# Kernel tuning notes

Hardware: AMD Instinct MI355X
Metric: run time of the kernel (lower is better)

The kernel has to match this reference:

```python
import jax, jax.numpy as jnp
import numpy as np
import math

B, S, D, H = 2, 2048, 1024, 16
HD = D // H  # 64


def setup_inputs() -> dict:
    key = jax.random.key(0)
    ks = jax.random.split(key, 12)
    s = 1.0 / math.sqrt(D)
    inp = {
        "x": jax.random.normal(ks[0], (B, S, D), dtype=jnp.float32),
        "Wq": jax.random.normal(ks[1], (D, D), dtype=jnp.float32) * s,
        "bq": jnp.zeros((D,), dtype=jnp.float32),
        "Wk": jax.random.normal(ks[2], (D, D), dtype=jnp.float32) * s,
        "bk": jnp.zeros((D,), dtype=jnp.float32),
        "Wv": jax.random.normal(ks[3], (D, D), dtype=jnp.float32) * s,
        "bv": jnp.zeros((D,), dtype=jnp.float32),
        "Wo": jax.random.normal(ks[4], (D, D), dtype=jnp.float32) * s,
        "bo": jnp.zeros((D,), dtype=jnp.float32),
        "cross_modal_weights": jnp.ones((3, 3), dtype=jnp.float32),
        "mask": jax.random.randint(ks[5], (B, S, S), 0, 2, dtype=jnp.int32),
        "modality_info": jax.random.randint(ks[6], (B, S), 0, 3, dtype=jnp.int64),
    }
    return inp


def reference(x, Wq, bq, Wk, bk, Wv, bv, Wo, bo, cross_modal_weights, mask, modality_info):
    b, s, d = x.shape
    # QKV projections -> [b, H, s, HD]
    q = (x @ Wq + bq).reshape(b, s, H, HD).transpose(0, 2, 1, 3)
    k = (x @ Wk + bk).reshape(b, s, H, HD).transpose(0, 2, 1, 3)
    v = (x @ Wv + bv).reshape(b, s, H, HD).transpose(0, 2, 1, 3)
    scores = jnp.einsum("bhqd,bhkd->bhqk", q, k) / math.sqrt(HD)
    # modality bias: torch uses .item() -> detached scalar
    modality_bias = jax.lax.stop_gradient(jnp.mean(cross_modal_weights))
    scores = scores + modality_bias
    # user mask [b, s, s] broadcast over heads; masked_fill(mask==0, -1e9)
    scores = jnp.where(mask[:, None, :, :] == 0, jnp.float32(-1e9), scores)
    attn = jax.nn.softmax(scores, axis=-1)
    # dropout_rate = 0.0 (eval) -> identity
    ctx = jnp.einsum("bhqk,bhkd->bhqd", attn, v)
    ctx = ctx.transpose(0, 2, 1, 3).reshape(b, s, d)
    return ctx @ Wo + bo
```

## Files before the change

### kernel.cpp

```cpp
#include <hip/hip_runtime.h>
#include <math.h>

#define Bdim 2
#define Sdim 2048
#define Ddim 1024
#define Hnum 16
#define HDdim 64
#define Kdim 1024

using short8   = __attribute__((ext_vector_type(8))) short;
using ushort8  = __attribute__((ext_vector_type(8))) unsigned short;
using ushort4v = __attribute__((ext_vector_type(4))) unsigned short;
using floatx4  = __attribute__((ext_vector_type(4))) float;
using half4    = __attribute__((ext_vector_type(4))) _Float16;
using half2v   = __attribute__((ext_vector_type(2))) _Float16;

__device__ __forceinline__ unsigned short f2bf(float f) {
    __bf16 b = (__bf16)f;
    return __builtin_bit_cast(unsigned short, b);
}

__device__ __forceinline__ void async_ld16(const unsigned short* g, unsigned short* l) {
    __builtin_amdgcn_global_load_lds(
        (const __attribute__((address_space(1))) unsigned int*)(g),
        (__attribute__((address_space(3))) unsigned int*)(l), 16, 0, 0);
}

__global__ __launch_bounds__(256) void prep_kernel(
    const float* __restrict__ x,
    const float* __restrict__ Wq, const float* __restrict__ Wk,
    const float* __restrict__ Wv, const float* __restrict__ Wo,
    const int* __restrict__ mask,
    unsigned short* __restrict__ xb, unsigned short* __restrict__ Wt,
    unsigned long long* __restrict__ packed)
{
    __shared__ float tile[64][65];
    const int bid = blockIdx.x;
    const int t   = threadIdx.x;

    if (bid < 2048) {
        size_t i = ((size_t)bid * 256 + t) * 8;
        float4 a = *(const float4*)(x + i);
        float4 b = *(const float4*)(x + i + 4);
        ushort8 o;
        o[0] = f2bf(a.x); o[1] = f2bf(a.y); o[2] = f2bf(a.z); o[3] = f2bf(a.w);
        o[4] = f2bf(b.x); o[5] = f2bf(b.y); o[6] = f2bf(b.z); o[7] = f2bf(b.w);
        *(ushort8*)(xb + i) = o;
    } else if (bid < 3072) {
        const int idx = bid - 2048;
        const int n0 = (idx & 15) * 64;
        const int k0 = ((idx >> 4) & 15) * 64;
        const int z  = idx >> 8;
        const float* W = (z == 0) ? Wq : (z == 1) ? Wk : (z == 2) ? Wv : Wo;
        unsigned short* outp = Wt + (size_t)z * Kdim * Ddim;
#pragma unroll
        for (int i = 0; i < 4; ++i) {
            int flat = i * 256 + t;
            int r = flat >> 4;
            int c = (flat & 15) * 4;
            float4 v = *(const float4*)(W + (size_t)(k0 + r) * Ddim + n0 + c);
            tile[r][c] = v.x; tile[r][c+1] = v.y; tile[r][c+2] = v.z; tile[r][c+3] = v.w;
        }
        __syncthreads();
#pragma unroll
        for (int i = 0; i < 16; ++i) {
            int flat = i * 256 + t;
            int n = flat >> 6;
            int k = flat & 63;
            outp[(size_t)(n0 + n) * Kdim + k0 + k] = f2bf(tile[k][n]);
        }
    } else {
        const int lane = t & 63;
        const int l15  = lane & 15;
        const int quad = lane >> 4;
        const unsigned int gid = (bid - 3072) * 4 + (t >> 6);
        const int b  = gid >> 14;
        const int qg = (gid >> 7) & 127;
        const int kb = gid & 127;
        int4 mv = *(const int4*)(mask + ((size_t)(b * Sdim) + qg * 16 + l15) * Sdim + kb * 16 + quad * 4);
        unsigned long long w0 = __ballot(mv.x != 0);
        unsigned long long w1 = __ballot(mv.y != 0);
        unsigned long long w2 = __ballot(mv.z != 0);
        unsigned long long w3 = __ballot(mv.w != 0);
        if (lane == 0) {
            unsigned long long* dst = packed + (size_t)gid * 4;
            dst[0] = w0; dst[1] = w1; dst[2] = w2; dst[3] = w3;
        }
    }
}

#define MFMA_NORM(MT, NT) acc[MT][NT] = __builtin_amdgcn_mfma_f32_16x16x32_bf16(af[MT], bfr[NT], acc[MT][NT], 0, 0, 0)
#define MFMA_SWAP(MT, NT) acc[MT][NT] = __builtin_amdgcn_mfma_f32_16x16x32_bf16(bfr[NT], af[MT], acc[MT][NT], 0, 0, 0)

#define GEMM_KLOOP(APTR, WPTR, NT_TILES, MFMA_STMT)                              \
    for (int kt = 0; kt < 16; ++kt) {                                            \
        const int k0 = kt * 64;                                                  \
        __syncthreads();                                                         \
        _Pragma("unroll")                                                        \
        for (int i = 0; i < 4; ++i) {                                            \
            int flat = i * 256 + t;                                              \
            int row  = flat >> 3;                                                \
            int cg   = (flat & 7) ^ (row & 7);                                   \
            async_ld16(APTR + (size_t)(m0 + row) * Kdim + k0 + cg * 8,           \
                       As + flat * 8);                                           \
        }                                                                        \
        _Pragma("unroll")                                                        \
        for (int i = 0; i < NT_TILES; ++i) {                                     \
            int flat = i * 256 + t;                                              \
            int row  = flat >> 3;                                                \
            int cg   = (flat & 7) ^ (row & 7);                                   \
            async_ld16(WPTR + (size_t)row * Kdim + k0 + cg * 8,                  \
                       Bs + flat * 8);                                           \
        }                                                                        \
        __syncthreads();                                                         \
        _Pragma("unroll")                                                        \
        for (int ks = 0; ks < 2; ++ks) {                                         \
            short8 af[4], bfr[NT_TILES];                                         \
            _Pragma("unroll")                                                    \
            for (int mt = 0; mt < 4; ++mt) {                                     \
                int row = wm * 64 + mt * 16 + l15;                               \
                int ch  = (ks * 4 + quad) ^ (row & 7);                           \
                af[mt] = *(const short8*)(As + row * 64 + ch * 8);               \
            }                                                                    \
            _Pragma("unroll")                                                    \
            for (int nt = 0; nt < NT_TILES; ++nt) {                              \
                int row = wn * (NT_TILES * 16) + nt * 16 + l15;                  \
                int ch  = (ks * 4 + quad) ^ (row & 7);                           \
                bfr[nt] = *(const short8*)(Bs + row * 64 + ch * 8);              \
            }                                                                    \
            _Pragma("unroll")                                                    \
            for (int mt = 0; mt < 4; ++mt)                                       \
                _Pragma("unroll")                                                \
                for (int nt = 0; nt < NT_TILES; ++nt)                            \
                    MFMA_STMT(mt, nt);                                           \
        }                                                                        \
    }

__global__ __launch_bounds__(256) void qkv_mfma_kernel(
    const unsigned short* __restrict__ A, const unsigned short* __restrict__ Wt,
    const float* __restrict__ bq, const float* __restrict__ bk, const float* __restrict__ bv,
    unsigned short* __restrict__ qo, unsigned short* __restrict__ ko, _Float16* __restrict__ vto)
{
    __shared__ __align__(16) unsigned short As[128 * 64];
    __shared__ __align__(16) unsigned short Bs[128 * 64];
    const int n0   = blockIdx.x * 128;
    const int m0   = blockIdx.y * 128;
    const int wsel = n0 >> 10;
    const int c0   = n0 & 1023;
    const unsigned short* Wp = Wt + (size_t)wsel * Kdim * Ddim + (size_t)c0 * Kdim;

    const int t    = threadIdx.x;
    const int lane = t & 63;
    const int w    = t >> 6;
    const int quad = lane >> 4;
    const int l15  = lane & 15;
    const int wm   = w & 1;
    const int wn   = w >> 1;
    floatx4 acc[4][4];
#pragma unroll
    for (int mt = 0; mt < 4; ++mt)
#pragma unroll
        for (int nt = 0; nt < 4; ++nt) acc[mt][nt] = (floatx4){0.f, 0.f, 0.f, 0.f};

    if (wsel < 2) {
        GEMM_KLOOP(A, Wp, 4, MFMA_SWAP)
        const float* bias = wsel ? bk : bq;
        unsigned short* outp = wsel ? ko : qo;
        const float qsc = wsel ? 1.0f : 0.18033688011112042f;
#pragma unroll
        for (int mt = 0; mt < 4; ++mt) {
            int m    = m0 + wm * 64 + mt * 16 + l15;
            int bidx = m >> 11;
            int s    = m & 2047;
#pragma unroll
            for (int nt = 0; nt < 4; ++nt) {
                int c = c0 + wn * 64 + nt * 16 + quad * 4;
                float4 bb = *(const float4*)(bias + c);
                int h  = c >> 6;
                int hd = c & 63;
                ushort4v o;
                o[0] = f2bf((acc[mt][nt][0] + bb.x) * qsc);
                o[1] = f2bf((acc[mt][nt][1] + bb.y) * qsc);
                o[2] = f2bf((acc[mt][nt][2] + bb.z) * qsc);
                o[3] = f2bf((acc[mt][nt][3] + bb.w) * qsc);
                *(ushort4v*)(outp + ((size_t)(bidx * Hnum + h) * Sdim + s) * HDdim + hd) = o;
            }
        }
    } else {
        GEMM_KLOOP(A, Wp, 4, MFMA_NORM)
#pragma unroll
        for (int nt = 0; nt < 4; ++nt) {
            int c = c0 + wn * 64 + nt * 16 + l15;
            float bb = bv[c];
            int h  = c >> 6;
            int hd = c & 63;
#pragma unroll
            for (int mt = 0; mt < 4; ++mt) {
                int m    = m0 + wm * 64 + mt * 16 + quad * 4;
                int bidx = m >> 11;
                int s    = m & 2047;
                half4 o;
#pragma unroll
                for (int r = 0; r < 4; ++r) o[r] = (_Float16)(acc[mt][nt][r] + bb);
                *(half4*)(vto + ((size_t)(bidx * Hnum + h) * HDdim + hd) * Sdim + s) = o;
            }
        }
    }
}

__global__ __launch_bounds__(256) void out_mfma_kernel(
    const unsigned short* __restrict__ A, const unsigned short* __restrict__ Wt,
    const float* __restrict__ bias, float* __restrict__ out)
{
    __shared__ __align__(16) unsigned short As[128 * 64];
    __shared__ __align__(16) unsigned short Bs[64 * 64];
    const int n0 = blockIdx.x * 64;
    const int m0 = blockIdx.y * 128;
    const unsigned short* Wp = Wt + (size_t)3 * Kdim * Ddim + (size_t)n0 * Kdim;

    const int t    = threadIdx.x;
    const int lane = t & 63;
    const int w    = t >> 6;
    const int quad = lane >> 4;
    const int l15  = lane & 15;
    const int wm   = w & 1;
    const int wn   = w >> 1;
    floatx4 acc[4][2];
#pragma unroll
    for (int mt = 0; mt < 4; ++mt)
#pragma unroll
        for (int nt = 0; nt < 2; ++nt) acc[mt][nt] = (floatx4){0.f, 0.f, 0.f, 0.f};

    GEMM_KLOOP(A, Wp, 2, MFMA_SWAP)

#pragma unroll
    for (int mt = 0; mt < 4; ++mt) {
        int m = m0 + wm * 64 + mt * 16 + l15;
#pragma unroll
        for (int nt = 0; nt < 2; ++nt) {
            int c = n0 + wn * 32 + nt * 16 + quad * 4;
            float4 bb = *(const float4*)(bias + c);
            float4 o = make_float4(acc[mt][nt][0] + bb.x, acc[mt][nt][1] + bb.y,
                                   acc[mt][nt][2] + bb.z, acc[mt][nt][3] + bb.w);
            *(float4*)(out + (size_t)m * Ddim + c) = o;
        }
    }
}

__global__ __launch_bounds__(256, 2) void attn_mfma_kernel(
    const unsigned short* __restrict__ q, const unsigned short* __restrict__ k,
    const _Float16* __restrict__ vt, const unsigned long long* __restrict__ pmask,
    unsigned short* __restrict__ ctx)
{
    __shared__ __align__(16) unsigned short Ks[2][64 * 64];
    __shared__ __align__(16) _Float16       Vs[2][64 * 64];

    const int t    = threadIdx.x;
    const int w    = t >> 6;
    const int lane = t & 63;
    const int quad = lane >> 4;
    const int l15  = lane & 15;
    const int bid  = blockIdx.x;
    const int bh   = bid & 31;
    const int qseg = bid >> 5;
    const int b    = bh >> 4;
    const int h    = bh & 15;
    const int qrow0 = qseg * 128 + w * 32;

    const unsigned short* qp = q  + (size_t)bh * Sdim * HDdim;
    const unsigned short* kp = k  + (size_t)bh * Sdim * HDdim;
    const _Float16*       vp = vt + (size_t)bh * HDdim * Sdim;

    const int qg0 = __builtin_amdgcn_readfirstlane(qrow0 >> 4);
    const unsigned long long* __restrict__ pm =
        pmask + ((size_t)(b * 128 + qg0) * 128) * 4;

    short8 qf[2][2];
#pragma unroll
    for (int g = 0; g < 2; ++g)
#pragma unroll
        for (int ks = 0; ks < 2; ++ks)
            qf[g][ks] = *(const short8*)(qp + (size_t)(qrow0 + g * 16 + l15) * HDdim + ks * 32 + quad * 8);

    floatx4 acc[2][4];
    floatx4 accl[2];
#pragma unroll
    for (int g = 0; g < 2; ++g) {
        accl[g] = (floatx4){0.f, 0.f, 0.f, 0.f};
#pragma unroll
        for (int hs = 0; hs < 4; ++hs) acc[g][hs] = (floatx4){0.f, 0.f, 0.f, 0.f};
    }
    const half4 ones = {(_Float16)1.f, (_Float16)1.f, (_Float16)1.f, (_Float16)1.f};

    auto stage = [&](int buf, int key0) {
#pragma unroll
        for (int i = 0; i < 2; ++i) {
            int flat = i * 256 + t;
            int row  = flat >> 3;
            int cg   = (flat & 7) ^ (row & 7);
            async_ld16(kp + (size_t)(key0 + row) * HDdim + cg * 8, &Ks[buf][flat * 8]);
        }
#pragma unroll
        for (int i = 0; i < 2; ++i) {
            int flat = i * 256 + t;
            int row  = flat >> 3;
            int cg   = (flat & 7) ^ (row & 7);
            async_ld16((const unsigned short*)(vp + (size_t)row * Sdim + key0 + cg * 8),
                       (unsigned short*)&Vs[buf][flat * 8]);
        }
    };

    stage(0, 0);

#pragma unroll 2
    for (int kt = 0; kt < 32; ++kt) {
        const int cur = kt & 1;
        __syncthreads();
        if (kt < 31) stage(cur ^ 1, (kt + 1) * 64);

        short8 kf[2][4];
#pragma unroll
        for (int ks = 0; ks < 2; ++ks)
#pragma unroll
            for (int sub = 0; sub < 4; ++sub) {
                int row = sub * 16 + l15;
                int ch  = (ks * 4 + quad) ^ (row & 7);
                kf[ks][sub] = *(const short8*)&Ks[cur][row * 64 + ch * 8];
            }
        half4 vf[4][4];
#pragma unroll
        for (int hs = 0; hs < 4; ++hs)
#pragma unroll
            for (int c = 0; c < 4; ++c) {
                int row = hs * 16 + l15;
                int cc  = c * 2 + (quad >> 1);
                int ch  = cc ^ (row & 7);
                vf[hs][c] = *(const half4*)&Vs[cur][row * 64 + ch * 8 + (quad & 1) * 4];
            }

        floatx4 sc[2][4];
#pragma unroll
        for (int g = 0; g < 2; ++g)
#pragma unroll
            for (int sub = 0; sub < 4; ++sub) sc[g][sub] = (floatx4){0.f, 0.f, 0.f, 0.f};
#pragma unroll
        for (int ks = 0; ks < 2; ++ks)
#pragma unroll
            for (int sub = 0; sub < 4; ++sub)
#pragma unroll
                for (int g = 0; g < 2; ++g)
                    sc[g][sub] = __builtin_amdgcn_mfma_f32_16x16x32_bf16(
                        kf[ks][sub], qf[g][ks], sc[g][sub], 0, 0, 0);

        half4 pf[2][4];
#pragma unroll
        for (int g = 0; g < 2; ++g) {
            const unsigned long long* __restrict__ pg = pm + g * 512 + kt * 16;
#pragma unroll
            for (int c = 0; c < 4; ++c) {
                float pv[4];
#pragma unroll
                for (int r = 0; r < 4; ++r) {
                    float p = exp2f(sc[g][c][r]);
                    unsigned long long wmask = pg[c * 4 + r];
                    asm("v_cndmask_b32 %0, 0, %1, %2" : "=v"(pv[r]) : "v"(p), "s"(wmask));
                }
                half2v lo = __builtin_bit_cast(half2v, __builtin_amdgcn_cvt_pkrtz(pv[0], pv[1]));
                half2v hi = __builtin_bit_cast(half2v, __builtin_amdgcn_cvt_pkrtz(pv[2], pv[3]));
                pf[g][c][0] = lo[0]; pf[g][c][1] = lo[1];
                pf[g][c][2] = hi[0]; pf[g][c][3] = hi[1];
            }
        }

#pragma unroll
        for (int c = 0; c < 4; ++c) {
#pragma unroll
            for (int hs = 0; hs < 4; ++hs)
#pragma unroll
                for (int g = 0; g < 2; ++g)
                    acc[g][hs] = __builtin_amdgcn_mfma_f32_16x16x16f16(
                        vf[hs][c], pf[g][c], acc[g][hs], 0, 0, 0);
#pragma unroll
            for (int g = 0; g < 2; ++g)
                accl[g] = __builtin_amdgcn_mfma_f32_16x16x16f16(
                    ones, pf[g][c], accl[g], 0, 0, 0);
        }
    }

#pragma unroll
    for (int g = 0; g < 2; ++g) {
        float inv = 1.0f / fmaxf(accl[g][0], 1e-30f);
        int row = qrow0 + g * 16 + l15;
#pragma unroll
        for (int hs = 0; hs < 4; ++hs) {
            ushort4v o;
#pragma unroll
            for (int r = 0; r < 4; ++r) o[r] = f2bf(acc[g][hs][r] * inv);
            *(ushort4v*)(ctx + (size_t)(b * Sdim + row) * Ddim + h * 64 + hs * 16 + quad * 4) = o;
        }
    }
}

extern "C" void kernel_launch(void* const* d_in, const int* in_sizes, int n_in,
                              void* d_out, int out_size, void* d_ws, size_t ws_size,
                              hipStream_t stream) {
    const float* x   = (const float*)d_in[0];
    const float* Wq  = (const float*)d_in[1];
    const float* bq  = (const float*)d_in[2];
    const float* Wk  = (const float*)d_in[3];
    const float* bk  = (const float*)d_in[4];
    const float* Wv  = (const float*)d_in[5];
    const float* bv  = (const float*)d_in[6];
    const float* Wo  = (const float*)d_in[7];
    const float* bo  = (const float*)d_in[8];
    const int*  mask = (const int*)d_in[10];
    float* out = (float*)d_out;

    char* ws = (char*)d_ws;
    unsigned short* xb  = (unsigned short*)(ws);
    unsigned short* Wt  = (unsigned short*)(ws + (size_t)8  * 1048576);
    unsigned short* qb  = (unsigned short*)(ws + (size_t)16 * 1048576);
    unsigned short* kb  = (unsigned short*)(ws + (size_t)24 * 1048576);
    _Float16*       vtb = (_Float16*)     (ws + (size_t)32 * 1048576);
    unsigned long long* pmk = (unsigned long long*)(ws + (size_t)40 * 1048576);
    unsigned short* ctxb = xb;

    prep_kernel<<<dim3(11264), 256, 0, stream>>>(x, Wq, Wk, Wv, Wo, mask, xb, Wt, pmk);
    qkv_mfma_kernel<<<dim3(24, 32), 256, 0, stream>>>(xb, Wt, bq, bk, bv, qb, kb, vtb);
    attn_mfma_kernel<<<dim3(512), 256, 0, stream>>>(qb, kb, vtb, pmk, ctxb);
    out_mfma_kernel<<<dim3(16, 32), 256, 0, stream>>>(ctxb, Wt, bo, out);
}
```

Baseline: 250.9 us.

## Split attention key tiles across wave pairs and reduce partial sums in LDS

Each attention block now covers 64 query rows instead of 128. Its four waves form two query groups times two key halves, and each wave processes half of every 64-key tile. The grid doubles to 1024 blocks and launch bounds rise to 4 blocks per CU, which lowers per-wave register pressure and increases occupancy and parallelism. The cost is a cross-wave reduction of the output and row-sum accumulators through LDS at the end, and each K/V tile staged in shared memory now feeds half as many query rows.

```diff
diff --git a/kernel.cpp b/kernel.cpp
--- a/kernel.cpp
+++ b/kernel.cpp
@@ -247,7 +247,7 @@
     }
 }
 
-__global__ __launch_bounds__(256, 2) void attn_mfma_kernel(
+__global__ __launch_bounds__(256, 4) void attn_mfma_kernel(
     const unsigned short* __restrict__ q, const unsigned short* __restrict__ k,
     const _Float16* __restrict__ vt, const unsigned long long* __restrict__ pmask,
     unsigned short* __restrict__ ctx)
@@ -265,15 +265,18 @@
     const int qseg = bid >> 5;
     const int b    = bh >> 4;
     const int h    = bh & 15;
-    const int qrow0 = qseg * 128 + w * 32;
+    const int wq   = w & 1;
+    const int wk   = w >> 1;
+    const int qrow0 = qseg * 64 + wq * 32;
 
     const unsigned short* qp = q  + (size_t)bh * Sdim * HDdim;
     const unsigned short* kp = k  + (size_t)bh * Sdim * HDdim;
     const _Float16*       vp = vt + (size_t)bh * HDdim * Sdim;
 
     const int qg0 = __builtin_amdgcn_readfirstlane(qrow0 >> 4);
+    const int wku = __builtin_amdgcn_readfirstlane(wk);
     const unsigned long long* __restrict__ pm =
-        pmask + ((size_t)(b * 128 + qg0) * 128) * 4;
+        pmask + ((size_t)(b * 128 + qg0) * 128) * 4 + wku * 8;
 
     short8 qf[2][2];
 #pragma unroll
@@ -318,46 +321,46 @@
         __syncthreads();
         if (kt < 31) stage(cur ^ 1, (kt + 1) * 64);
 
-        short8 kf[2][4];
+        short8 kf[2][2];
 #pragma unroll
         for (int ks = 0; ks < 2; ++ks)
 #pragma unroll
-            for (int sub = 0; sub < 4; ++sub) {
-                int row = sub * 16 + l15;
+            for (int sub = 0; sub < 2; ++sub) {
+                int row = wk * 32 + sub * 16 + l15;
                 int ch  = (ks * 4 + quad) ^ (row & 7);
                 kf[ks][sub] = *(const short8*)&Ks[cur][row * 64 + ch * 8];
             }
-        half4 vf[4][4];
+        half4 vf[4][2];
 #pragma unroll
         for (int hs = 0; hs < 4; ++hs)
 #pragma unroll
-            for (int c = 0; c < 4; ++c) {
+            for (int c = 0; c < 2; ++c) {
                 int row = hs * 16 + l15;
-                int cc  = c * 2 + (quad >> 1);
+                int cc  = (wk * 2 + c) * 2 + (quad >> 1);
                 int ch  = cc ^ (row & 7);
                 vf[hs][c] = *(const half4*)&Vs[cur][row * 64 + ch * 8 + (quad & 1) * 4];
             }
 
-        floatx4 sc[2][4];
+        floatx4 sc[2][2];
 #pragma unroll
         for (int g = 0; g < 2; ++g)
 #pragma unroll
-            for (int sub = 0; sub < 4; ++sub) sc[g][sub] = (floatx4){0.f, 0.f, 0.f, 0.f};
+            for (int sub = 0; sub < 2; ++sub) sc[g][sub] = (floatx4){0.f, 0.f, 0.f, 0.f};
 #pragma unroll
         for (int ks = 0; ks < 2; ++ks)
 #pragma unroll
-            for (int sub = 0; sub < 4; ++sub)
+            for (int sub = 0; sub < 2; ++sub)
 #pragma unroll
                 for (int g = 0; g < 2; ++g)
                     sc[g][sub] = __builtin_amdgcn_mfma_f32_16x16x32_bf16(
                         kf[ks][sub], qf[g][ks], sc[g][sub], 0, 0, 0);
 
-        half4 pf[2][4];
+        half4 pf[2][2];
 #pragma unroll
         for (int g = 0; g < 2; ++g) {
             const unsigned long long* __restrict__ pg = pm + g * 512 + kt * 16;
 #pragma unroll
-            for (int c = 0; c < 4; ++c) {
+            for (int c = 0; c < 2; ++c) {
                 float pv[4];
 #pragma unroll
                 for (int r = 0; r < 4; ++r) {
@@ -373,7 +376,7 @@
         }
 
 #pragma unroll
-        for (int c = 0; c < 4; ++c) {
+        for (int c = 0; c < 2; ++c) {
 #pragma unroll
             for (int hs = 0; hs < 4; ++hs)
 #pragma unroll
@@ -387,16 +390,33 @@
         }
     }
 
-#pragma unroll
-    for (int g = 0; g < 2; ++g) {
-        float inv = 1.0f / fmaxf(accl[g][0], 1e-30f);
-        int row = qrow0 + g * 16 + l15;
-#pragma unroll
-        for (int hs = 0; hs < 4; ++hs) {
-            ushort4v o;
-#pragma unroll
-            for (int r = 0; r < 4; ++r) o[r] = f2bf(acc[g][hs][r] * inv);
-            *(ushort4v*)(ctx + (size_t)(b * Sdim + row) * Ddim + h * 64 + hs * 16 + quad * 4) = o;
+    __syncthreads();
+    float* red  = (float*)&Ks[0][0];
+    float* redl = (float*)&Vs[0][0];
+    if (wk == 1) {
+#pragma unroll
+        for (int g = 0; g < 2; ++g) {
+#pragma unroll
+            for (int hs = 0; hs < 4; ++hs)
+                *(floatx4*)&red[((((wq * 2) + g) * 4 + hs) * 64 + lane) * 4] = acc[g][hs];
+            redl[(wq * 2 + g) * 64 + lane] = accl[g][0];
+        }
+    }
+    __syncthreads();
+    if (wk == 0) {
+#pragma unroll
+        for (int g = 0; g < 2; ++g) {
+            float lsum = accl[g][0] + redl[(wq * 2 + g) * 64 + lane];
+            float inv  = 1.0f / fmaxf(lsum, 1e-30f);
+            int row = qrow0 + g * 16 + l15;
+#pragma unroll
+            for (int hs = 0; hs < 4; ++hs) {
+                floatx4 o4 = acc[g][hs] + *(const floatx4*)&red[((((wq * 2) + g) * 4 + hs) * 64 + lane) * 4];
+                ushort4v o;
+#pragma unroll
+                for (int r = 0; r < 4; ++r) o[r] = f2bf(o4[r] * inv);
+                *(ushort4v*)(ctx + (size_t)(b * Sdim + row) * Ddim + h * 64 + hs * 16 + quad * 4) = o;
+            }
         }
     }
 }
@@ -427,6 +447,6 @@
 
     prep_kernel<<<dim3(11264), 256, 0, stream>>>(x, Wq, Wk, Wv, Wo, mask, xb, Wt, pmk);
     qkv_mfma_kernel<<<dim3(24, 32), 256, 0, stream>>>(xb, Wt, bq, bk, bv, qb, kb, vtb);
-    attn_mfma_kernel<<<dim3(512), 256, 0, stream>>>(qb, kb, vtb, pmk, ctxb);
+    attn_mfma_kernel<<<dim3(1024), 256, 0, stream>>>(qb, kb, vtb, pmk, ctxb);
     out_mfma_kernel<<<dim3(16, 32), 256, 0, stream>>>(ctxb, Wt, bo, out);
 }
```

New measurement: 245.9 us. -2.0%, faster.
